# Performance work log

Hardware: AMD Instinct MI355X
Metric: run time of the kernel (lower is better)

The kernel has to match this reference:

```python
import jax, jax.numpy as jnp
import numpy as np

B, S, D, H = 2, 2048, 1024, 16
DK = D // H
NEG = -1e9


def setup_inputs() -> dict:
    key = jax.random.key(0)
    ks = jax.random.split(key, 12)
    scale = 1.0 / np.sqrt(D)
    inp = {
        'Q': jax.random.normal(ks[0], (B, S, D), jnp.float32),
        'K': jax.random.normal(ks[1], (B, S, D), jnp.float32),
        'V': jax.random.normal(ks[2], (B, S, D), jnp.float32),
        'mask': jnp.tril(jnp.ones((S, S), jnp.int32))[None, None],  # (1,1,S,S) causal
        # torch nn.Linear layout: W has shape (out, in), y = x @ W.T + b
        'WQ': jax.random.normal(ks[3], (D, D), jnp.float32) * scale,
        'bQ': jnp.zeros((D,), jnp.float32),
        'WK': jax.random.normal(ks[4], (D, D), jnp.float32) * scale,
        'bK': jnp.zeros((D,), jnp.float32),
        'WV': jax.random.normal(ks[5], (D, D), jnp.float32) * scale,
        'bV': jnp.zeros((D,), jnp.float32),
        'WO': jax.random.normal(ks[6], (D, D), jnp.float32) * scale,
        'bO': jnp.zeros((D,), jnp.float32),
    }
    return inp


def reference(Q, K, V, mask, WQ, bQ, WK, bK, WV, bV, WO, bO):
    # projections (torch Linear: x @ W.T + b), then split heads -> (B,H,S,DK)
    def split_heads(x):
        return x.reshape(B, S, H, DK).transpose(0, 2, 1, 3)

    Qh = split_heads(Q @ WQ.T + bQ)
    Kh = split_heads(K @ WK.T + bK)
    Vh = split_heads(V @ WV.T + bV)

    scores = jnp.einsum('bhqd,bhkd->bhqk', Qh, Kh) / jnp.sqrt(jnp.float32(DK))
    scores = jnp.where(mask == 0, NEG, scores)
    attn = jax.nn.softmax(scores, axis=-1)  # (B,H,S,S)
    ctx = jnp.einsum('bhqk,bhkd->bhqd', attn, Vh)
    concat = ctx.transpose(0, 2, 1, 3).reshape(B, S, D)
    out = concat @ WO.T + bO
    return out, attn
```

## Files before the change

### kernel.cpp

```cpp
#include <hip/hip_runtime.h>
#include <hip/hip_bf16.h>
#include <cstdint>
#include <cstddef>

#define S_ 2048
#define D_ 1024
#define H_ 16
#define DK_ 64
#define B_ 2

typedef unsigned short u16;
typedef __attribute__((ext_vector_type(8))) short bf16x8;
typedef __attribute__((ext_vector_type(4))) float f32x4;

__device__ inline u16 f2bf(float f) {
    union { float f; unsigned u; } c; c.f = f;
    unsigned u = c.u;
    unsigned r = (u + 0x7fffu + ((u >> 16) & 1u)) >> 16;
    return (u16)r;
}

__device__ inline uint4 cvt8(const float* __restrict__ src) {
    float4 f0 = *(const float4*)(src);
    float4 f1 = *(const float4*)(src + 4);
    union { u16 h[8]; uint4 v; } u;
    u.h[0] = f2bf(f0.x); u.h[1] = f2bf(f0.y); u.h[2] = f2bf(f0.z); u.h[3] = f2bf(f0.w);
    u.h[4] = f2bf(f1.x); u.h[5] = f2bf(f1.y); u.h[6] = f2bf(f1.z); u.h[7] = f2bf(f1.w);
    return u.v;
}

template<int BM, int BN, int MODE, bool AF32, bool BF32, bool CF32>
__global__ void __launch_bounds__(256)
gemm_bt(const void* __restrict__ Av, const void* __restrict__ Bv,
        const float* __restrict__ bias, void* __restrict__ Cv,
        int M, int N, int K, int lda, int ldb)
{
    constexpr int BK  = 32;
    constexpr int BKP = 40;
    constexpr int WN = BN / 64;
    constexpr int WM = 4 / WN;
    static_assert(BM == WM * 64, "tile/wave mismatch");

    __shared__ __align__(16) u16 As[BM * BKP];
    __shared__ __align__(16) u16 Bs[BN * BKP];

    const int tid  = threadIdx.x;
    const int lane = tid & 63;
    const int wave = tid >> 6;
    const int wm = wave / WN;
    const int wn = wave % WN;
    const int m0 = blockIdx.y * BM;
    const int n0 = blockIdx.x * BN;

    const float* Af = (const float*)Av;
    const u16*   Ab = (const u16*)Av;
    const float* Bf = (const float*)Bv;
    const u16*   Bb = (const u16*)Bv;

    f32x4 acc[4][4];
#pragma unroll
    for (int i = 0; i < 4; ++i)
#pragma unroll
        for (int j = 0; j < 4; ++j)
            acc[i][j] = (f32x4){0.f, 0.f, 0.f, 0.f};

    const int fr = lane & 15;
    const int fk = (lane >> 4) << 3;

    for (int k0 = 0; k0 < K; k0 += BK) {
#pragma unroll
        for (int i = 0; i < BM / 64; ++i) {
            int linear = i * 256 + tid;
            int row = linear >> 2;
            int kk  = (linear & 3) << 3;
            size_t off = (size_t)(m0 + row) * lda + k0 + kk;
            *(uint4*)&As[row * BKP + kk] =
                AF32 ? cvt8(&Af[off]) : *(const uint4*)&Ab[off];
        }
#pragma unroll
        for (int i = 0; i < BN / 64; ++i) {
            int linear = i * 256 + tid;
            int row = linear >> 2;
            int kk  = (linear & 3) << 3;
            size_t off = (size_t)(n0 + row) * ldb + k0 + kk;
            *(uint4*)&Bs[row * BKP + kk] =
                BF32 ? cvt8(&Bf[off]) : *(const uint4*)&Bb[off];
        }
        __syncthreads();

        bf16x8 af[4], bfv[4];
#pragma unroll
        for (int mt = 0; mt < 4; ++mt)
            af[mt] = *(const bf16x8*)&As[(wm * 64 + mt * 16 + fr) * BKP + fk];
#pragma unroll
        for (int nt = 0; nt < 4; ++nt)
            bfv[nt] = *(const bf16x8*)&Bs[(wn * 64 + nt * 16 + fr) * BKP + fk];
#pragma unroll
        for (int mt = 0; mt < 4; ++mt)
#pragma unroll
            for (int nt = 0; nt < 4; ++nt)
                acc[mt][nt] = __builtin_amdgcn_mfma_f32_16x16x32_bf16(
                    af[mt], bfv[nt], acc[mt][nt], 0, 0, 0);
        __syncthreads();
    }

#pragma unroll
    for (int mt = 0; mt < 4; ++mt) {
#pragma unroll
        for (int nt = 0; nt < 4; ++nt) {
#pragma unroll
            for (int r = 0; r < 4; ++r) {
                int row = m0 + wm * 64 + mt * 16 + ((lane >> 4) << 2) + r;
                int col = n0 + wn * 64 + nt * 16 + (lane & 15);
                float v = acc[mt][nt][r];
                if (bias) v += bias[col];
                size_t addr;
                if (MODE == 0) {
                    addr = (size_t)row * N + col;
                } else if (MODE == 1) {
                    addr = ((size_t)(row >> 11) << 21) + ((size_t)(col >> 6) << 17)
                         + ((size_t)(row & 2047) << 6) + (size_t)(col & 63);
                } else {
                    addr = ((size_t)(row >> 11) << 21) + ((size_t)(col >> 6) << 17)
                         + ((size_t)(col & 63) << 11) + (size_t)(row & 2047);
                }
                if (CF32) ((float*)Cv)[addr] = v;
                else      ((u16*)Cv)[addr]   = f2bf(v);
            }
        }
    }
}

__global__ void __launch_bounds__(256)
attn_sums(const u16* __restrict__ Qh, const u16* __restrict__ Kh,
          float* __restrict__ sums)
{
    __shared__ __align__(16) u16 Qs[128 * 64];
    __shared__ __align__(16) u16 Ks[128 * 64];
    __shared__ float rowsum[128];

    const int tid  = threadIdx.x;
    const int lane = tid & 63;
    const int wave = tid >> 6;
    const int wm = wave >> 1, wn = wave & 1;
    const int qt = blockIdx.x;
    const int bh = blockIdx.y;

    const u16* Qbase = Qh + (size_t)bh * S_ * DK_ + (size_t)qt * 128 * DK_;
    const u16* Kbase = Kh + (size_t)bh * S_ * DK_;

#pragma unroll
    for (int i = 0; i < 4; ++i) {
        int linear = i * 256 + tid;
        int row = linear >> 3;
        *(uint4*)((char*)Qs + (row << 7) + ((((linear & 7) << 4)) ^ ((row & 7) << 4)))
            = *(const uint4*)&Qbase[(size_t)linear << 3];
    }
    if (tid < 128) rowsum[tid] = 0.f;

    float rs[4][4];
#pragma unroll
    for (int i = 0; i < 4; ++i)
#pragma unroll
        for (int j = 0; j < 4; ++j) rs[i][j] = 0.f;

    const int fr = lane & 15;
    const int fq = lane >> 4;

    for (int kt = 0; kt <= qt; ++kt) {
        __syncthreads();
#pragma unroll
        for (int i = 0; i < 4; ++i) {
            int linear = i * 256 + tid;
            int row = linear >> 3;
            *(uint4*)((char*)Ks + (row << 7) + ((((linear & 7) << 4)) ^ ((row & 7) << 4)))
                = *(const uint4*)&Kbase[(size_t)kt * 128 * DK_ + ((size_t)linear << 3)];
        }
        __syncthreads();

        f32x4 acc[4][4];
#pragma unroll
        for (int i = 0; i < 4; ++i)
#pragma unroll
            for (int j = 0; j < 4; ++j) acc[i][j] = (f32x4){0.f, 0.f, 0.f, 0.f};

#pragma unroll
        for (int ks = 0; ks < 64; ks += 32) {
            bf16x8 af[4], bfv[4];
#pragma unroll
            for (int mt = 0; mt < 4; ++mt) {
                int row = wm * 64 + mt * 16 + fr;
                af[mt] = *(const bf16x8*)((const char*)Qs + (row << 7)
                          + ((((ks + (fq << 3)) << 1)) ^ ((row & 7) << 4)));
            }
#pragma unroll
            for (int nt = 0; nt < 4; ++nt) {
                int row = wn * 64 + nt * 16 + fr;
                bfv[nt] = *(const bf16x8*)((const char*)Ks + (row << 7)
                          + ((((ks + (fq << 3)) << 1)) ^ ((row & 7) << 4)));
            }
#pragma unroll
            for (int mt = 0; mt < 4; ++mt)
#pragma unroll
                for (int nt = 0; nt < 4; ++nt)
                    acc[mt][nt] = __builtin_amdgcn_mfma_f32_16x16x32_bf16(
                        af[mt], bfv[nt], acc[mt][nt], 0, 0, 0);
        }

        const bool diag = (kt == qt);
#pragma unroll
        for (int mt = 0; mt < 4; ++mt)
#pragma unroll
            for (int nt = 0; nt < 4; ++nt)
#pragma unroll
                for (int r = 0; r < 4; ++r) {
                    int row = wm * 64 + mt * 16 + (fq << 2) + r;
                    int col = wn * 64 + nt * 16 + fr;
                    if (!diag || col <= row)
                        rs[mt][r] += __expf(acc[mt][nt][r] * 0.125f);
                }
    }

#pragma unroll
    for (int mt = 0; mt < 4; ++mt)
#pragma unroll
        for (int r = 0; r < 4; ++r) {
            float v = rs[mt][r];
            v += __shfl_xor(v, 1, 64);
            v += __shfl_xor(v, 2, 64);
            v += __shfl_xor(v, 4, 64);
            v += __shfl_xor(v, 8, 64);
            rs[mt][r] = v;
        }
    __syncthreads();
    if (fr == 0) {
#pragma unroll
        for (int mt = 0; mt < 4; ++mt)
#pragma unroll
            for (int r = 0; r < 4; ++r)
                atomicAdd(&rowsum[wm * 64 + mt * 16 + (fq << 2) + r], rs[mt][r]);
    }
    __syncthreads();
    if (tid < 128)
        sums[(size_t)bh * S_ + (size_t)qt * 128 + tid] = rowsum[tid];
}

__global__ void __launch_bounds__(256, 2)
attn_fused(const u16* __restrict__ Qh, const u16* __restrict__ Kh,
           const u16* __restrict__ Vt, const float* __restrict__ sums,
           float* __restrict__ attn, u16* __restrict__ Cc)
{
    __shared__ __align__(16) u16 Qs[128 * 64];
    __shared__ __align__(16) u16 Ks[128 * 64];
    __shared__ __align__(16) u16 Vs[64 * 128];
    __shared__ __align__(16) u16 Ps[128 * 128];

    const int tid  = threadIdx.x;
    const int lane = tid & 63;
    const int wave = tid >> 6;
    const int wm = wave >> 1, wn = wave & 1;
    const int qt = blockIdx.x;
    const int bh = blockIdx.y;
    const int fr = lane & 15;
    const int fq = lane >> 4;

    const u16* Qbase = Qh + (size_t)bh * S_ * DK_ + (size_t)qt * 128 * DK_;
    const u16* Kbase = Kh + (size_t)bh * S_ * DK_;
    const u16* Vbase = Vt + (size_t)bh * (size_t)DK_ * S_;
    float* out = attn + (size_t)bh * S_ * S_;

#pragma unroll
    for (int i = 0; i < 4; ++i) {
        int linear = i * 256 + tid;
        int row = linear >> 3;
        *(uint4*)((char*)Qs + (row << 7) + ((((linear & 7) << 4)) ^ ((row & 7) << 4)))
            = *(const uint4*)&Qbase[(size_t)linear << 3];
    }

    float rcp[4][4];
#pragma unroll
    for (int mt = 0; mt < 4; ++mt)
#pragma unroll
        for (int r = 0; r < 4; ++r) {
            int grow = qt * 128 + wm * 64 + mt * 16 + (fq << 2) + r;
            rcp[mt][r] = 1.0f / sums[(size_t)bh * S_ + grow];
        }

    f32x4 cacc[4][2];
#pragma unroll
    for (int i = 0; i < 4; ++i)
#pragma unroll
        for (int j = 0; j < 2; ++j) cacc[i][j] = (f32x4){0.f, 0.f, 0.f, 0.f};

    for (int kt = 0; kt <= qt; ++kt) {
        __syncthreads();
#pragma unroll
        for (int i = 0; i < 4; ++i) {
            int linear = i * 256 + tid;
            int row = linear >> 3;
            *(uint4*)((char*)Ks + (row << 7) + ((((linear & 7) << 4)) ^ ((row & 7) << 4)))
                = *(const uint4*)&Kbase[(size_t)kt * 128 * DK_ + ((size_t)linear << 3)];
        }
#pragma unroll
        for (int i = 0; i < 4; ++i) {
            int linear = i * 256 + tid;
            int row = linear >> 4;
            int cb  = (linear & 15) << 4;
            *(uint4*)((char*)Vs + (row << 8) + (cb ^ ((row & 7) << 4)))
                = *(const uint4*)&Vbase[(size_t)row * S_ + kt * 128 + ((linear & 15) << 3)];
        }
        __syncthreads();

        f32x4 acc[4][4];
#pragma unroll
        for (int i = 0; i < 4; ++i)
#pragma unroll
            for (int j = 0; j < 4; ++j) acc[i][j] = (f32x4){0.f, 0.f, 0.f, 0.f};

#pragma unroll
        for (int ks = 0; ks < 64; ks += 32) {
            bf16x8 af[4], bfv[4];
#pragma unroll
            for (int mt = 0; mt < 4; ++mt) {
                int row = wm * 64 + mt * 16 + fr;
                af[mt] = *(const bf16x8*)((const char*)Qs + (row << 7)
                          + ((((ks + (fq << 3)) << 1)) ^ ((row & 7) << 4)));
            }
#pragma unroll
            for (int nt = 0; nt < 4; ++nt) {
                int row = wn * 64 + nt * 16 + fr;
                bfv[nt] = *(const bf16x8*)((const char*)Ks + (row << 7)
                          + ((((ks + (fq << 3)) << 1)) ^ ((row & 7) << 4)));
            }
#pragma unroll
            for (int mt = 0; mt < 4; ++mt)
#pragma unroll
                for (int nt = 0; nt < 4; ++nt)
                    acc[mt][nt] = __builtin_amdgcn_mfma_f32_16x16x32_bf16(
                        af[mt], bfv[nt], acc[mt][nt], 0, 0, 0);
        }

        const bool diag = (kt == qt);
#pragma unroll
        for (int mt = 0; mt < 4; ++mt)
#pragma unroll
            for (int nt = 0; nt < 4; ++nt)
#pragma unroll
                for (int r = 0; r < 4; ++r) {
                    int row = wm * 64 + mt * 16 + (fq << 2) + r;
                    int col = wn * 64 + nt * 16 + fr;
                    float p = 0.f;
                    if (!diag || col <= row)
                        p = __expf(acc[mt][nt][r] * 0.125f) * rcp[mt][r];
                    out[(size_t)(qt * 128 + row) * S_ + kt * 128 + col] = p;
                    *(u16*)((char*)Ps + (row << 8) + (((col << 1)) ^ ((row & 7) << 4)))
                        = f2bf(p);
                }
        __syncthreads();

#pragma unroll
        for (int ks4 = 0; ks4 < 4; ++ks4) {
            bf16x8 pf[4], vf[2];
            int kb = (ks4 * 32 + (fq << 3)) << 1;
#pragma unroll
            for (int mt = 0; mt < 4; ++mt) {
                int row = wm * 64 + mt * 16 + fr;
                pf[mt] = *(const bf16x8*)((const char*)Ps + (row << 8)
                          + (kb ^ ((row & 7) << 4)));
            }
#pragma unroll
            for (int nt = 0; nt < 2; ++nt) {
                int row = wn * 32 + nt * 16 + fr;
                vf[nt] = *(const bf16x8*)((const char*)Vs + (row << 8)
                          + (kb ^ ((row & 7) << 4)));
            }
#pragma unroll
            for (int mt = 0; mt < 4; ++mt)
#pragma unroll
                for (int nt = 0; nt < 2; ++nt)
                    cacc[mt][nt] = __builtin_amdgcn_mfma_f32_16x16x32_bf16(
                        pf[mt], vf[nt], cacc[mt][nt], 0, 0, 0);
        }
    }

#pragma unroll
    for (int mt = 0; mt < 4; ++mt)
#pragma unroll
        for (int nt = 0; nt < 2; ++nt)
#pragma unroll
            for (int r = 0; r < 4; ++r) {
                int row = wm * 64 + mt * 16 + (fq << 2) + r;
                int col = wn * 32 + nt * 16 + fr;
                size_t addr = (size_t)(bh >> 4) * S_ * D_ + (size_t)(bh & 15) * DK_
                            + (size_t)(qt * 128 + row) * D_ + col;
                Cc[addr] = f2bf(cacc[mt][nt][r]);
            }

    float4 z4 = {0.f, 0.f, 0.f, 0.f};
    for (int kt2 = qt + 1; kt2 < S_ / 128; ++kt2) {
#pragma unroll
        for (int i = 0; i < 16; ++i) {
            int linear = i * 256 + tid;
            int row = linear >> 5;
            int c   = (linear & 31) << 2;
            *(float4*)&out[(size_t)(qt * 128 + row) * S_ + kt2 * 128 + c] = z4;
        }
    }
}

extern "C" void kernel_launch(void* const* d_in, const int* in_sizes, int n_in,
                              void* d_out, int out_size, void* d_ws, size_t ws_size,
                              hipStream_t stream)
{
    const float* Q  = (const float*)d_in[0];
    const float* K  = (const float*)d_in[1];
    const float* V  = (const float*)d_in[2];
    const float* WQ = (const float*)d_in[4];
    const float* bQ = (const float*)d_in[5];
    const float* WK = (const float*)d_in[6];
    const float* bK = (const float*)d_in[7];
    const float* WV = (const float*)d_in[8];
    const float* bV = (const float*)d_in[9];
    const float* WO = (const float*)d_in[10];
    const float* bO = (const float*)d_in[11];

    float* outF  = (float*)d_out;
    float* attnF = outF + (size_t)B_ * S_ * D_;

    u16* Qh = (u16*)d_ws;
    u16* Kh = Qh + (size_t)B_ * S_ * D_;
    u16* Vt = Kh + (size_t)B_ * S_ * D_;
    u16* Cc = Vt + (size_t)B_ * S_ * D_;
    float* sums = (float*)(Cc + (size_t)B_ * S_ * D_);

    dim3 blk(256, 1, 1);
    const int M = B_ * S_;

    gemm_bt<128, 128, 1, true, true, false>
        <<<dim3(D_ / 128, M / 128, 1), blk, 0, stream>>>(
        Q, WQ, bQ, Qh, M, D_, D_, D_, D_);
    gemm_bt<128, 128, 1, true, true, false>
        <<<dim3(D_ / 128, M / 128, 1), blk, 0, stream>>>(
        K, WK, bK, Kh, M, D_, D_, D_, D_);
    gemm_bt<128, 128, 2, true, true, false>
        <<<dim3(D_ / 128, M / 128, 1), blk, 0, stream>>>(
        V, WV, bV, Vt, M, D_, D_, D_, D_);

    attn_sums<<<dim3(S_ / 128, B_ * H_, 1), blk, 0, stream>>>(Qh, Kh, sums);

    attn_fused<<<dim3(S_ / 128, B_ * H_, 1), blk, 0, stream>>>(
        Qh, Kh, Vt, sums, attnF, Cc);

    gemm_bt<128, 128, 0, false, true, true>
        <<<dim3(D_ / 128, M / 128, 1), blk, 0, stream>>>(
        Cc, WO, bO, outF, M, D_, D_, D_, D_);
}
```

Before: 924.1 us.

## Merge QKV projections into one launch and fuse row-sum pass into attention

The three Q/K/V projection GEMMs become a single launch that selects its operands by blockIdx.z. The separate row-sum kernel is folded into the attention kernel: each block first computes its softmax denominators into shared memory (aliased onto the P buffer), then does the main pass. This removes the global round-trip for the sums. Query tiles are also interleaved (0,15,1,14,…) so long and short causal tiles are paired, balancing load across the grid. Costs: fewer launches and better triangle balance, but the attention blocks now carry both passes, so less parallelism overlaps the row-sum work.

```diff
diff --git a/kernel.cpp b/kernel.cpp
--- a/kernel.cpp
+++ b/kernel.cpp
@@ -29,31 +29,112 @@
     return u.v;
 }
 
-template<int BM, int BN, int MODE, bool AF32, bool BF32, bool CF32>
 __global__ void __launch_bounds__(256)
-gemm_bt(const void* __restrict__ Av, const void* __restrict__ Bv,
-        const float* __restrict__ bias, void* __restrict__ Cv,
+proj_qkv(const float* __restrict__ Qi, const float* __restrict__ Ki,
+         const float* __restrict__ Vi,
+         const float* __restrict__ WQ, const float* __restrict__ WK,
+         const float* __restrict__ WV,
+         const float* __restrict__ bQ, const float* __restrict__ bK,
+         const float* __restrict__ bV,
+         u16* __restrict__ Qo, u16* __restrict__ Ko, u16* __restrict__ Vo)
+{
+    constexpr int BK  = 32;
+    constexpr int BKP = 40;
+
+    __shared__ __align__(16) u16 As[128 * BKP];
+    __shared__ __align__(16) u16 Bs[128 * BKP];
+
+    const int tid  = threadIdx.x;
+    const int lane = tid & 63;
+    const int wave = tid >> 6;
+    const int wm = wave >> 1;
+    const int wn = wave & 1;
+    const int m0 = blockIdx.y * 128;
+    const int n0 = blockIdx.x * 128;
+    const int z  = blockIdx.z;
+
+    const float* A    = (z == 0) ? Qi : (z == 1) ? Ki : Vi;
+    const float* W    = (z == 0) ? WQ : (z == 1) ? WK : WV;
+    const float* bias = (z == 0) ? bQ : (z == 1) ? bK : bV;
+    u16*         O    = (z == 0) ? Qo : (z == 1) ? Ko : Vo;
+
+    f32x4 acc[4][4];
+#pragma unroll
+    for (int i = 0; i < 4; ++i)
+#pragma unroll
+        for (int j = 0; j < 4; ++j)
+            acc[i][j] = (f32x4){0.f, 0.f, 0.f, 0.f};
+
+    const int fr = lane & 15;
+    const int fk = (lane >> 4) << 3;
+
+    for (int k0 = 0; k0 < D_; k0 += BK) {
+#pragma unroll
+        for (int i = 0; i < 2; ++i) {
+            int linear = i * 256 + tid;
+            int row = linear >> 2;
+            int kk  = (linear & 3) << 3;
+            *(uint4*)&As[row * BKP + kk] = cvt8(&A[(size_t)(m0 + row) * D_ + k0 + kk]);
+            *(uint4*)&Bs[row * BKP + kk] = cvt8(&W[(size_t)(n0 + row) * D_ + k0 + kk]);
+        }
+        __syncthreads();
+
+        bf16x8 af[4], bfv[4];
+#pragma unroll
+        for (int mt = 0; mt < 4; ++mt)
+            af[mt] = *(const bf16x8*)&As[(wm * 64 + mt * 16 + fr) * BKP + fk];
+#pragma unroll
+        for (int nt = 0; nt < 4; ++nt)
+            bfv[nt] = *(const bf16x8*)&Bs[(wn * 64 + nt * 16 + fr) * BKP + fk];
+#pragma unroll
+        for (int mt = 0; mt < 4; ++mt)
+#pragma unroll
+            for (int nt = 0; nt < 4; ++nt)
+                acc[mt][nt] = __builtin_amdgcn_mfma_f32_16x16x32_bf16(
+                    af[mt], bfv[nt], acc[mt][nt], 0, 0, 0);
+        __syncthreads();
+    }
+
+#pragma unroll
+    for (int mt = 0; mt < 4; ++mt)
+#pragma unroll
+        for (int nt = 0; nt < 4; ++nt)
+#pragma unroll
+            for (int r = 0; r < 4; ++r) {
+                int row = m0 + wm * 64 + mt * 16 + ((lane >> 4) << 2) + r;
+                int col = n0 + wn * 64 + nt * 16 + (lane & 15);
+                float v = acc[mt][nt][r] + bias[col];
+                size_t addr;
+                if (z < 2)
+                    addr = ((size_t)(row >> 11) << 21) + ((size_t)(col >> 6) << 17)
+                         + ((size_t)(row & 2047) << 6) + (size_t)(col & 63);
+                else
+                    addr = ((size_t)(row >> 11) << 21) + ((size_t)(col >> 6) << 17)
+                         + ((size_t)(col & 63) << 11) + (size_t)(row & 2047);
+                O[addr] = f2bf(v);
+            }
+}
+
+template<bool BF32>
+__global__ void __launch_bounds__(256)
+gemm_bt(const u16* __restrict__ Ab, const void* __restrict__ Bv,
+        const float* __restrict__ bias, float* __restrict__ C,
         int M, int N, int K, int lda, int ldb)
 {
     constexpr int BK  = 32;
     constexpr int BKP = 40;
-    constexpr int WN = BN / 64;
-    constexpr int WM = 4 / WN;
-    static_assert(BM == WM * 64, "tile/wave mismatch");
-
-    __shared__ __align__(16) u16 As[BM * BKP];
-    __shared__ __align__(16) u16 Bs[BN * BKP];
+
+    __shared__ __align__(16) u16 As[128 * BKP];
+    __shared__ __align__(16) u16 Bs[128 * BKP];
 
     const int tid  = threadIdx.x;
     const int lane = tid & 63;
     const int wave = tid >> 6;
-    const int wm = wave / WN;
-    const int wn = wave % WN;
-    const int m0 = blockIdx.y * BM;
-    const int n0 = blockIdx.x * BN;
-
-    const float* Af = (const float*)Av;
-    const u16*   Ab = (const u16*)Av;
+    const int wm = wave >> 1;
+    const int wn = wave & 1;
+    const int m0 = blockIdx.y * 128;
+    const int n0 = blockIdx.x * 128;
+
     const float* Bf = (const float*)Bv;
     const u16*   Bb = (const u16*)Bv;
 
@@ -69,22 +150,15 @@
 
     for (int k0 = 0; k0 < K; k0 += BK) {
 #pragma unroll
-        for (int i = 0; i < BM / 64; ++i) {
+        for (int i = 0; i < 2; ++i) {
             int linear = i * 256 + tid;
             int row = linear >> 2;
             int kk  = (linear & 3) << 3;
-            size_t off = (size_t)(m0 + row) * lda + k0 + kk;
             *(uint4*)&As[row * BKP + kk] =
-                AF32 ? cvt8(&Af[off]) : *(const uint4*)&Ab[off];
-        }
-#pragma unroll
-        for (int i = 0; i < BN / 64; ++i) {
-            int linear = i * 256 + tid;
-            int row = linear >> 2;
-            int kk  = (linear & 3) << 3;
-            size_t off = (size_t)(n0 + row) * ldb + k0 + kk;
+                *(const uint4*)&Ab[(size_t)(m0 + row) * lda + k0 + kk];
             *(uint4*)&Bs[row * BKP + kk] =
-                BF32 ? cvt8(&Bf[off]) : *(const uint4*)&Bb[off];
+                BF32 ? cvt8(&Bf[(size_t)(n0 + row) * ldb + k0 + kk])
+                     : *(const uint4*)&Bb[(size_t)(n0 + row) * ldb + k0 + kk];
         }
         __syncthreads();
 
@@ -105,49 +179,42 @@
     }
 
 #pragma unroll
-    for (int mt = 0; mt < 4; ++mt) {
-#pragma unroll
-        for (int nt = 0; nt < 4; ++nt) {
+    for (int mt = 0; mt < 4; ++mt)
+#pragma unroll
+        for (int nt = 0; nt < 4; ++nt)
 #pragma unroll
             for (int r = 0; r < 4; ++r) {
                 int row = m0 + wm * 64 + mt * 16 + ((lane >> 4) << 2) + r;
                 int col = n0 + wn * 64 + nt * 16 + (lane & 15);
-                float v = acc[mt][nt][r];
-                if (bias) v += bias[col];
-                size_t addr;
-                if (MODE == 0) {
-                    addr = (size_t)row * N + col;
-                } else if (MODE == 1) {
-                    addr = ((size_t)(row >> 11) << 21) + ((size_t)(col >> 6) << 17)
-                         + ((size_t)(row & 2047) << 6) + (size_t)(col & 63);
-                } else {
-                    addr = ((size_t)(row >> 11) << 21) + ((size_t)(col >> 6) << 17)
-                         + ((size_t)(col & 63) << 11) + (size_t)(row & 2047);
-                }
-                if (CF32) ((float*)Cv)[addr] = v;
-                else      ((u16*)Cv)[addr]   = f2bf(v);
-            }
-        }
-    }
-}
-
-__global__ void __launch_bounds__(256)
-attn_sums(const u16* __restrict__ Qh, const u16* __restrict__ Kh,
-          float* __restrict__ sums)
+                C[(size_t)row * N + col] = acc[mt][nt][r] + bias[col];
+            }
+}
+
+__global__ void __launch_bounds__(256, 2)
+attn_all(const u16* __restrict__ Qh, const u16* __restrict__ Kh,
+         const u16* __restrict__ Vt,
+         float* __restrict__ attn, u16* __restrict__ Cc)
 {
     __shared__ __align__(16) u16 Qs[128 * 64];
     __shared__ __align__(16) u16 Ks[128 * 64];
-    __shared__ float rowsum[128];
+    __shared__ __align__(16) u16 Vs[64 * 128];
+    __shared__ __align__(16) u16 Ps[128 * 128];
+    float* rowsum = (float*)Ps;
 
     const int tid  = threadIdx.x;
     const int lane = tid & 63;
     const int wave = tid >> 6;
     const int wm = wave >> 1, wn = wave & 1;
-    const int qt = blockIdx.x;
+    const int bx = blockIdx.x;
+    const int qt = (bx & 1) ? (15 - (bx >> 1)) : (bx >> 1);
     const int bh = blockIdx.y;
+    const int fr = lane & 15;
+    const int fq = lane >> 4;
 
     const u16* Qbase = Qh + (size_t)bh * S_ * DK_ + (size_t)qt * 128 * DK_;
     const u16* Kbase = Kh + (size_t)bh * S_ * DK_;
+    const u16* Vbase = Vt + (size_t)bh * (size_t)DK_ * S_;
+    float* out = attn + (size_t)bh * S_ * S_;
 
 #pragma unroll
     for (int i = 0; i < 4; ++i) {
@@ -163,9 +230,6 @@
     for (int i = 0; i < 4; ++i)
 #pragma unroll
         for (int j = 0; j < 4; ++j) rs[i][j] = 0.f;
-
-    const int fr = lane & 15;
-    const int fq = lane >> 4;
 
     for (int kt = 0; kt <= qt; ++kt) {
         __syncthreads();
@@ -241,50 +305,13 @@
                 atomicAdd(&rowsum[wm * 64 + mt * 16 + (fq << 2) + r], rs[mt][r]);
     }
     __syncthreads();
-    if (tid < 128)
-        sums[(size_t)bh * S_ + (size_t)qt * 128 + tid] = rowsum[tid];
-}
-
-__global__ void __launch_bounds__(256, 2)
-attn_fused(const u16* __restrict__ Qh, const u16* __restrict__ Kh,
-           const u16* __restrict__ Vt, const float* __restrict__ sums,
-           float* __restrict__ attn, u16* __restrict__ Cc)
-{
-    __shared__ __align__(16) u16 Qs[128 * 64];
-    __shared__ __align__(16) u16 Ks[128 * 64];
-    __shared__ __align__(16) u16 Vs[64 * 128];
-    __shared__ __align__(16) u16 Ps[128 * 128];
-
-    const int tid  = threadIdx.x;
-    const int lane = tid & 63;
-    const int wave = tid >> 6;
-    const int wm = wave >> 1, wn = wave & 1;
-    const int qt = blockIdx.x;
-    const int bh = blockIdx.y;
-    const int fr = lane & 15;
-    const int fq = lane >> 4;
-
-    const u16* Qbase = Qh + (size_t)bh * S_ * DK_ + (size_t)qt * 128 * DK_;
-    const u16* Kbase = Kh + (size_t)bh * S_ * DK_;
-    const u16* Vbase = Vt + (size_t)bh * (size_t)DK_ * S_;
-    float* out = attn + (size_t)bh * S_ * S_;
-
-#pragma unroll
-    for (int i = 0; i < 4; ++i) {
-        int linear = i * 256 + tid;
-        int row = linear >> 3;
-        *(uint4*)((char*)Qs + (row << 7) + ((((linear & 7) << 4)) ^ ((row & 7) << 4)))
-            = *(const uint4*)&Qbase[(size_t)linear << 3];
-    }
 
     float rcp[4][4];
 #pragma unroll
     for (int mt = 0; mt < 4; ++mt)
 #pragma unroll
-        for (int r = 0; r < 4; ++r) {
-            int grow = qt * 128 + wm * 64 + mt * 16 + (fq << 2) + r;
-            rcp[mt][r] = 1.0f / sums[(size_t)bh * S_ + grow];
-        }
+        for (int r = 0; r < 4; ++r)
+            rcp[mt][r] = 1.0f / rowsum[wm * 64 + mt * 16 + (fq << 2) + r];
 
     f32x4 cacc[4][2];
 #pragma unroll
@@ -431,27 +458,16 @@
     u16* Kh = Qh + (size_t)B_ * S_ * D_;
     u16* Vt = Kh + (size_t)B_ * S_ * D_;
     u16* Cc = Vt + (size_t)B_ * S_ * D_;
-    float* sums = (float*)(Cc + (size_t)B_ * S_ * D_);
 
     dim3 blk(256, 1, 1);
     const int M = B_ * S_;
 
-    gemm_bt<128, 128, 1, true, true, false>
-        <<<dim3(D_ / 128, M / 128, 1), blk, 0, stream>>>(
-        Q, WQ, bQ, Qh, M, D_, D_, D_, D_);
-    gemm_bt<128, 128, 1, true, true, false>
-        <<<dim3(D_ / 128, M / 128, 1), blk, 0, stream>>>(
-        K, WK, bK, Kh, M, D_, D_, D_, D_);
-    gemm_bt<128, 128, 2, true, true, false>
-        <<<dim3(D_ / 128, M / 128, 1), blk, 0, stream>>>(
-        V, WV, bV, Vt, M, D_, D_, D_, D_);
-
-    attn_sums<<<dim3(S_ / 128, B_ * H_, 1), blk, 0, stream>>>(Qh, Kh, sums);
-
-    attn_fused<<<dim3(S_ / 128, B_ * H_, 1), blk, 0, stream>>>(
-        Qh, Kh, Vt, sums, attnF, Cc);
-
-    gemm_bt<128, 128, 0, false, true, true>
-        <<<dim3(D_ / 128, M / 128, 1), blk, 0, stream>>>(
+    proj_qkv<<<dim3(D_ / 128, M / 128, 3), blk, 0, stream>>>(
+        Q, K, V, WQ, WK, WV, bQ, bK, bV, Qh, Kh, Vt);
+
+    attn_all<<<dim3(S_ / 128, B_ * H_, 1), blk, 0, stream>>>(
+        Qh, Kh, Vt, attnF, Cc);
+
+    gemm_bt<true><<<dim3(D_ / 128, M / 128, 1), blk, 0, stream>>>(
         Cc, WO, bO, outF, M, D_, D_, D_, D_);
 }
```

After: 806.9 us. -12.7%, faster.
